# Optimization experiments

Measured on AMD Instinct MI355X. Metric: run time of the kernel, lower is better.

## Reference

```python
import jax, jax.numpy as jnp
import numpy as np

B, NPG, EPG = 32768, 50, 400  # graphs, nodes/graph, edges/graph
N, E = B * NPG, B * EPG
BN_EPS = 1e-5


def setup_inputs() -> dict:
    key = jax.random.key(0)
    ks = jax.random.split(key, 16)
    # block-structured edges: endpoints local to each graph, then offset
    local = jax.random.randint(ks[0], (2, B, EPG), 0, NPG)
    offs = (jnp.arange(B, dtype=jnp.int32) * NPG)[None, :, None]
    edge_index = (local.astype(jnp.int32) + offs).reshape(2, E)
    x = jax.random.normal(ks[1], (N, 1), dtype=jnp.float32)
    s = 0.3
    inp = {
        "x": x, "edge_index": edge_index,
        "W11": s * jax.random.normal(ks[2], (1, 4)), "b11": jnp.zeros(4),
        "W21": s * jax.random.normal(ks[3], (4, 4)), "b21": jnp.zeros(4),
        "W12": s * jax.random.normal(ks[4], (1, 4)), "b12": jnp.zeros(4),
        "W22": s * jax.random.normal(ks[5], (4, 4)), "b22": jnp.zeros(4),
        "W13": s * jax.random.normal(ks[6], (1, 4)), "b13": jnp.zeros(4),
        "W23": s * jax.random.normal(ks[7], (4, 4)), "b23": jnp.zeros(4),
        "fc1_w": 0.05 * jax.random.normal(ks[8], (600, 16)), "fc1_b": jnp.zeros(16),
        "bn1_g": jnp.ones(16), "bn1_b": jnp.zeros(16),
        "fc2_w": 0.2 * jax.random.normal(ks[9], (16, 32)), "fc2_b": jnp.zeros(32),
        "bn2_g": jnp.ones(32), "bn2_b": jnp.zeros(32),
        "fc3_w": 0.2 * jax.random.normal(ks[10], (32, 2)), "fc3_b": jnp.zeros(2),
    }
    return inp


def _gcn_norm(edge_index, n):
    # add self-loops, symmetric D^{-1/2} A_hat D^{-1/2} normalization (PyG GCNConv)
    loop = jnp.arange(n, dtype=edge_index.dtype)
    src = jnp.concatenate([edge_index[0], loop])
    dst = jnp.concatenate([edge_index[1], loop])
    deg = jax.ops.segment_sum(jnp.ones_like(src, dtype=jnp.float32), dst, num_segments=n)
    dinv = jax.lax.rsqrt(jnp.maximum(deg, 1.0))  # deg >= 1 via self-loop
    return src, dst, dinv[src] * dinv[dst]


def _gcn(x, W, b, src, dst, norm, n):
    h = x @ W                                  # [N, out]
    msg = h[src] * norm[:, None]               # gather + scale
    return jax.ops.segment_sum(msg, dst, num_segments=n) + b  # scatter-add


def _bn(h, g, b):
    m = jnp.mean(h, axis=0)
    v = jnp.var(h, axis=0)  # biased, matches torch BN training forward
    return (h - m) * jax.lax.rsqrt(v + BN_EPS) * g + b


def reference(x, edge_index, W11, b11, W21, b21, W12, b12, W22, b22,
              W13, b13, W23, b23, fc1_w, fc1_b, bn1_g, bn1_b,
              fc2_w, fc2_b, bn2_g, bn2_b, fc3_w, fc3_b):
    n = x.shape[0]
    src, dst, norm = _gcn_norm(edge_index, n)
    x1 = _gcn(_gcn(x, W11, b11, src, dst, norm, n), W21, b21, src, dst, norm, n)
    x2 = _gcn(_gcn(x, W12, b12, src, dst, norm, n), W22, b22, src, dst, norm, n)
    x3 = _gcn(_gcn(x, W13, b13, src, dst, norm, n), W23, b23, src, dst, norm, n)
    h = jnp.concatenate([x1, x2, x3], axis=-1)          # [N, 12]
    h = h.reshape(n // NPG, NPG * 12)                   # [B, 600]
    h = _bn(jax.nn.relu(h @ fc1_w + fc1_b), bn1_g, bn1_b)
    h = _bn(jax.nn.relu(h @ fc2_w + fc2_b), bn2_g, bn2_b)
    return h @ fc3_w + fc3_b                            # [B, 2] logits
```

## Files before the change

kernel.cpp:

```cpp
#include <hip/hip_runtime.h>

#define NPG 50
#define EPG 400
#define NGRAPH 32768
#define NNODE (NGRAPH * NPG)
#define NEDGE (NGRAPH * EPG)
#define BN_EPS 1e-5f

#define WS_A1T 0
#define WS_A2T 1280
#define WS_K0 2560
#define WS_ST1 2576
#define WS_W2 2608
#define WS_B2 3120
#define WS_ST2 3152
#define WS_W3 3216
#define WS_B3 3280
#define WS_CNT1 3282
#define WS_CNT2 3283
#define WS_H1 4096

__global__ void FullGCN_52286931861996_kernel() {}

struct Params12 { const float* p[12]; };

__device__ __forceinline__ float rdlane(float v, int s) {
    return __uint_as_float(__builtin_amdgcn_readlane(__float_as_uint(v), s));
}

__global__ void k0_pre(Params12 wp, const float* __restrict__ fc1w,
                       const float* __restrict__ fc1b, float* __restrict__ ws) {
    __shared__ float U[12], C[12], Bc[12];
    int tid = threadIdx.x;
    if (tid < 12) {
        int b = tid >> 2, j = tid & 3;
        const float* W1 = wp.p[b * 4 + 0];
        const float* b1 = wp.p[b * 4 + 1];
        const float* W2 = wp.p[b * 4 + 2];
        const float* b2 = wp.p[b * 4 + 3];
        float u = 0.f, c = 0.f;
        for (int k = 0; k < 4; k++) {
            float w2 = W2[k * 4 + j];
            u += W1[k] * w2;
            c += b1[k] * w2;
        }
        U[tid] = u; C[tid] = c; Bc[tid] = b2[j];
    }
    __syncthreads();
    for (int idx = tid; idx < 2560; idx += blockDim.x) {
        int which = (idx >= 1280);
        int e = which ? idx - 1280 : idx;
        int l = e / 20, k = e % 20;
        int o = l >> 2, n = (l & 3) + 4 * k;
        const float* V = which ? C : U;
        float a = 0.f;
        if (k < 13 && n < NPG)
            for (int f = 0; f < 12; f++) a += V[f] * fc1w[(n * 12 + f) * 16 + o];
        ws[idx] = a;
    }
    if (tid < 16) {
        float a = fc1b[tid];
        for (int n = 0; n < NPG; n++)
            for (int f = 0; f < 12; f++)
                a += Bc[f] * fc1w[(n * 12 + f) * 16 + tid];
        ws[WS_K0 + tid] = a;
    }
    if (tid < 32) ws[WS_ST1 + tid] = 0.f;
    if (tid >= 64 && tid < 128) ws[WS_ST2 + (tid - 64)] = 0.f;
    if (tid == 200) { ((unsigned int*)ws)[WS_CNT1] = 0u; ((unsigned int*)ws)[WS_CNT2] = 0u; }
}

#define GPB 4
#define CROWW 13
#define CALLOC 840
#define CZERO 168
__global__ __launch_bounds__(256) void k1_gcn(const float* __restrict__ x,
                                              const int* __restrict__ edges,
                                              const float* __restrict__ ws,
                                              float* __restrict__ h1) {
    __shared__ unsigned int sC[GPB][CALLOC];
    __shared__ float2 sOut[GPB][64];

    int tid = threadIdx.x;
    int w = tid >> 6, lane = tid & 63;
    int g = blockIdx.x * GPB + w;
    int nb = g * NPG;
    unsigned int* sCw = &sC[w][0];

    {
        uint4 z = make_uint4(0u, 0u, 0u, 0u);
        uint4* cz = (uint4*)sCw;
        #pragma unroll
        for (int i = 0; i < 3; i++) {
            int j = lane + i * 64;
            if (j < CZERO) cz[j] = z;
        }
    }

    float xv = (lane < NPG) ? x[nb + lane] : 0.f;

    const int4* s4 = (const int4*)edges;
    const int4* d4 = s4 + (NEDGE / 4);
    int base = g * (EPG / 4);
    int4 sa = s4[base + lane];
    int4 da = d4[base + lane];
    bool m2 = lane < (EPG / 4 - 64);
    int4 sb = make_int4(0, 0, 0, 0), db = make_int4(0, 0, 0, 0);
    if (m2) { sb = s4[base + 64 + lane]; db = d4[base + 64 + lane]; }

    {
        int sl[8], dl[8];
        sl[0] = sa.x - nb; sl[1] = sa.y - nb; sl[2] = sa.z - nb; sl[3] = sa.w - nb;
        dl[0] = da.x - nb; dl[1] = da.y - nb; dl[2] = da.z - nb; dl[3] = da.w - nb;
        sl[4] = sb.x - nb; sl[5] = sb.y - nb; sl[6] = sb.z - nb; sl[7] = sb.w - nb;
        dl[4] = db.x - nb; dl[5] = db.y - nb; dl[6] = db.z - nb; dl[7] = db.w - nb;
        #pragma unroll
        for (int e = 0; e < 4; e++) {
            int cell = dl[e] * 52 + sl[e];
            atomicAdd(&sCw[cell >> 2], 1u << ((cell & 3) * 8));
        }
        if (m2) {
            #pragma unroll
            for (int e = 4; e < 8; e++) {
                int cell = dl[e] * 52 + sl[e];
                atomicAdd(&sCw[cell >> 2], 1u << ((cell & 3) * 8));
            }
        }
    }

    unsigned int wv[13];
    #pragma unroll
    for (int k = 0; k < 13; k++) wv[k] = sCw[lane * CROWW + k];

    unsigned int acc2 = 0;
    #pragma unroll
    for (int k = 0; k < 13; k++)
        acc2 += (wv[k] & 0x00FF00FFu) + ((wv[k] >> 8) & 0x00FF00FFu);
    int deg = 1 + (int)((acc2 & 0xFFFFu) + (acc2 >> 16));
    float dinv = rsqrtf((float)deg);
    float dd = dinv * dinv;
    float vs = dinv * xv;

    float pxa = 0.f, ra = 0.f;
    #pragma unroll
    for (int s = 0; s < NPG; s++) {
        float cnt = (float)((wv[s >> 2] >> ((s & 3) * 8)) & 0xFFu);
        pxa += cnt * rdlane(vs, s);
        ra  += cnt * rdlane(dinv, s);
    }
    float px = dinv * pxa + dd * xv;
    float rr = dinv * ra + dd;

    float vs2 = dinv * px;
    float ppa = 0.f;
    #pragma unroll
    for (int s = 0; s < NPG; s++) {
        float cnt = (float)((wv[s >> 2] >> ((s & 3) * 8)) & 0xFFu);
        ppa += cnt * rdlane(vs2, s);
    }
    float ppx = dinv * ppa + dd * px;

    if (lane >= NPG) { ppx = 0.f; rr = 0.f; }
    sOut[w][lane] = make_float2(ppx, rr);

    const float4* a1v = (const float4*)(ws + lane * 20);
    const float4* a2v = (const float4*)(ws + 1280 + lane * 20);
    float4 c0 = a1v[0], c1 = a1v[1], c2 = a1v[2];
    float  c3 = ws[lane * 20 + 12];
    float4 d0 = a2v[0], d1 = a2v[1], d2 = a2v[2];
    float  d3 = ws[1280 + lane * 20 + 12];
    float k0v = ws[WS_K0 + (lane >> 2)];
    float A1r[13] = {c0.x, c0.y, c0.z, c0.w, c1.x, c1.y, c1.z, c1.w, c2.x, c2.y, c2.z, c2.w, c3};
    float A2r[13] = {d0.x, d0.y, d0.z, d0.w, d1.x, d1.y, d1.z, d1.w, d2.x, d2.y, d2.z, d2.w, d3};

    int o = lane >> 2, q = lane & 3;
    float accz = 0.f;
    #pragma unroll
    for (int k = 0; k < 13; k++) {
        float2 pr = sOut[w][q + 4 * k];
        accz += pr.x * A1r[k] + pr.y * A2r[k];
    }
    accz += __shfl_down(accz, 2, 4);
    accz += __shfl_down(accz, 1, 4);
    if (q == 0) h1[(size_t)g * 16 + o] = fmaxf(accz + k0v, 0.f);
}

__global__ __launch_bounds__(256) void k23_stats_fold(const float* __restrict__ h1,
                                                      const float* __restrict__ fc2w,
                                                      const float* __restrict__ fc2b,
                                                      const float* __restrict__ g1,
                                                      const float* __restrict__ b1,
                                                      float* __restrict__ ws) {
    __shared__ float ps[32];
    __shared__ int last;
    int tid = threadIdx.x;
    if (tid < 32) ps[tid] = 0.f;
    __syncthreads();
    int c = tid & 15;
    float s = 0.f, sq = 0.f;
    for (int i = blockIdx.x * blockDim.x + tid; i < NGRAPH * 16; i += gridDim.x * blockDim.x) {
        float v = h1[i];
        s += v; sq += v * v;
    }
    s += __shfl_xor(s, 16); s += __shfl_xor(s, 32);
    sq += __shfl_xor(sq, 16); sq += __shfl_xor(sq, 32);
    if ((tid & 63) < 16) {
        atomicAdd(&ps[c], s);
        atomicAdd(&ps[16 + c], sq);
    }
    __syncthreads();
    if (tid < 32) atomicAdd(&ws[WS_ST1 + tid], ps[tid]);
    __threadfence();
    if (tid == 0)
        last = (atomicAdd(&((unsigned int*)ws)[WS_CNT1], 1u) == (unsigned int)(gridDim.x - 1));
    __syncthreads();
    if (!last) return;
    __threadfence();
    __shared__ float s1[16], t1[16];
    if (tid < 16) {
        float m  = atomicAdd(&ws[WS_ST1 + tid], 0.f) / (float)NGRAPH;
        float v  = atomicAdd(&ws[WS_ST1 + 16 + tid], 0.f) / (float)NGRAPH - m * m;
        float sc = g1[tid] * rsqrtf(v + BN_EPS);
        s1[tid] = sc;
        t1[tid] = b1[tid] - m * sc;
    }
    __syncthreads();
    for (int idx = tid; idx < 512; idx += blockDim.x)
        ws[WS_W2 + idx] = s1[idx >> 5] * fc2w[idx];
    if (tid < 32) {
        float a = fc2b[tid];
        for (int i = 0; i < 16; i++) a += t1[i] * fc2w[i * 32 + tid];
        ws[WS_B2 + tid] = a;
    }
}

__global__ __launch_bounds__(256) void k45_fc2_fold(const float* __restrict__ h1,
                                                    const float* __restrict__ fc3w,
                                                    const float* __restrict__ fc3b,
                                                    const float* __restrict__ g2,
                                                    const float* __restrict__ b2g,
                                                    float* __restrict__ ws) {
    __shared__ float w2[512];
    __shared__ float b2[32];
    __shared__ float pSum[32], pSq[32];
    __shared__ int last;
    int tid = threadIdx.x;
    for (int i = tid; i < 512; i += 256) w2[i] = ws[WS_W2 + i];
    if (tid < 32) {
        b2[tid] = ws[WS_B2 + tid];
        pSum[tid] = 0.f;
        pSq[tid] = 0.f;
    }
    __syncthreads();
    int g = blockIdx.x * blockDim.x + tid;
    int lane = tid & 63;
    const float4* h4 = (const float4*)(h1 + (size_t)g * 16);
    float4 a0 = h4[0], a1 = h4[1], a2 = h4[2], a3 = h4[3];
    float hin[16] = {a0.x, a0.y, a0.z, a0.w, a1.x, a1.y, a1.z, a1.w,
                     a2.x, a2.y, a2.z, a2.w, a3.x, a3.y, a3.z, a3.w};
    for (int o = 0; o < 32; o++) {
        float acc = b2[o];
        #pragma unroll
        for (int i = 0; i < 16; i++) acc += hin[i] * w2[i * 32 + o];
        acc = fmaxf(acc, 0.f);
        float v = acc, v2 = acc * acc;
        #pragma unroll
        for (int off = 32; off; off >>= 1) {
            v += __shfl_xor(v, off);
            v2 += __shfl_xor(v2, off);
        }
        if (lane == 0) {
            atomicAdd(&pSum[o], v);
            atomicAdd(&pSq[o], v2);
        }
    }
    __syncthreads();
    if (tid < 32) {
        atomicAdd(&ws[WS_ST2 + tid], pSum[tid]);
        atomicAdd(&ws[WS_ST2 + 32 + tid], pSq[tid]);
    }
    __threadfence();
    if (tid == 0)
        last = (atomicAdd(&((unsigned int*)ws)[WS_CNT2], 1u) == (unsigned int)(gridDim.x - 1));
    __syncthreads();
    if (!last) return;
    __threadfence();
    __shared__ float s2[32], t2[32];
    if (tid < 32) {
        float m  = atomicAdd(&ws[WS_ST2 + tid], 0.f) / (float)NGRAPH;
        float v  = atomicAdd(&ws[WS_ST2 + 32 + tid], 0.f) / (float)NGRAPH - m * m;
        float sc = g2[tid] * rsqrtf(v + BN_EPS);
        s2[tid] = sc;
        t2[tid] = b2g[tid] - m * sc;
    }
    __syncthreads();
    if (tid < 64) ws[WS_W3 + tid] = s2[tid >> 1] * fc3w[tid];
    if (tid < 2) {
        float a = fc3b[tid];
        for (int i = 0; i < 32; i++) a += t2[i] * fc3w[i * 2 + tid];
        ws[WS_B3 + tid] = a;
    }
}

__global__ __launch_bounds__(256) void k6_out(const float* __restrict__ h1,
                                              const float* __restrict__ ws,
                                              float2* __restrict__ out) {
    __shared__ float w2[512];
    __shared__ float b2[32];
    __shared__ float w3[64];
    __shared__ float b3[2];
    int tid = threadIdx.x;
    for (int i = tid; i < 512; i += 256) w2[i] = ws[WS_W2 + i];
    if (tid < 32) b2[tid] = ws[WS_B2 + tid];
    if (tid >= 64 && tid < 128) w3[tid - 64] = ws[WS_W3 + (tid - 64)];
    if (tid >= 128 && tid < 130) b3[tid - 128] = ws[WS_B3 + (tid - 128)];
    __syncthreads();
    int g = blockIdx.x * blockDim.x + tid;
    const float4* h4 = (const float4*)(h1 + (size_t)g * 16);
    float4 a0 = h4[0], a1 = h4[1], a2 = h4[2], a3 = h4[3];
    float hin[16] = {a0.x, a0.y, a0.z, a0.w, a1.x, a1.y, a1.z, a1.w,
                     a2.x, a2.y, a2.z, a2.w, a3.x, a3.y, a3.z, a3.w};
    float z0 = b3[0], z1 = b3[1];
    for (int o = 0; o < 32; o++) {
        float acc = b2[o];
        #pragma unroll
        for (int i = 0; i < 16; i++) acc += hin[i] * w2[i * 32 + o];
        acc = fmaxf(acc, 0.f);
        z0 += acc * w3[o * 2];
        z1 += acc * w3[o * 2 + 1];
    }
    out[g] = make_float2(z0, z1);
}

extern "C" void kernel_launch(void* const* d_in, const int* in_sizes, int n_in,
                              void* d_out, int out_size, void* d_ws, size_t ws_size,
                              hipStream_t stream) {
    (void)in_sizes; (void)n_in; (void)out_size; (void)ws_size;
    const float* x = (const float*)d_in[0];
    const int* edges = (const int*)d_in[1];
    Params12 wp;
    for (int i = 0; i < 12; i++) wp.p[i] = (const float*)d_in[2 + i];
    const float* fc1w = (const float*)d_in[14];
    const float* fc1b = (const float*)d_in[15];
    const float* bn1g = (const float*)d_in[16];
    const float* bn1b = (const float*)d_in[17];
    const float* fc2w = (const float*)d_in[18];
    const float* fc2b = (const float*)d_in[19];
    const float* bn2g = (const float*)d_in[20];
    const float* bn2b = (const float*)d_in[21];
    const float* fc3w = (const float*)d_in[22];
    const float* fc3b = (const float*)d_in[23];

    float* ws = (float*)d_ws;
    float* h1 = ws + WS_H1;

    k0_pre<<<1, 256, 0, stream>>>(wp, fc1w, fc1b, ws);
    k1_gcn<<<NGRAPH / GPB, 256, 0, stream>>>(x, edges, ws, h1);
    k23_stats_fold<<<256, 256, 0, stream>>>(h1, fc2w, fc2b, bn1g, bn1b, ws);
    k45_fc2_fold<<<NGRAPH / 256, 256, 0, stream>>>(h1, fc3w, fc3b, bn2g, bn2b, ws);
    k6_out<<<NGRAPH / 256, 256, 0, stream>>>(h1, ws, (float2*)d_out);
}
```

Measured before the change: 275.9 us.

## Fuse fc2 stats and output kernels via grid barrier; use LDS broadcast in GCN

Merges the fc2 BN-stats kernel and the final output kernel into a single launch. The last block to arrive computes the folded fc3 weights, and the other blocks spin on a counter flag before reading them. This removes one kernel launch and keeps h1 and w2 resident in registers. In the GCN kernel, the per-source lane reads (rdlane) are replaced by LDS broadcast reads, and the A-matrix loads are hoisted ahead of the edge processing. The spin barrier relies on all 128 blocks being co-resident, which holds at this grid size but adds a deadlock risk.

New measurement: 279.3 us. No clear change (+1.2%).

```diff
diff --git a/kernel.cpp b/kernel.cpp
--- a/kernel.cpp
+++ b/kernel.cpp
@@ -99,70 +99,6 @@
 
     float xv = (lane < NPG) ? x[nb + lane] : 0.f;
 
-    const int4* s4 = (const int4*)edges;
-    const int4* d4 = s4 + (NEDGE / 4);
-    int base = g * (EPG / 4);
-    int4 sa = s4[base + lane];
-    int4 da = d4[base + lane];
-    bool m2 = lane < (EPG / 4 - 64);
-    int4 sb = make_int4(0, 0, 0, 0), db = make_int4(0, 0, 0, 0);
-    if (m2) { sb = s4[base + 64 + lane]; db = d4[base + 64 + lane]; }
-
-    {
-        int sl[8], dl[8];
-        sl[0] = sa.x - nb; sl[1] = sa.y - nb; sl[2] = sa.z - nb; sl[3] = sa.w - nb;
-        dl[0] = da.x - nb; dl[1] = da.y - nb; dl[2] = da.z - nb; dl[3] = da.w - nb;
-        sl[4] = sb.x - nb; sl[5] = sb.y - nb; sl[6] = sb.z - nb; sl[7] = sb.w - nb;
-        dl[4] = db.x - nb; dl[5] = db.y - nb; dl[6] = db.z - nb; dl[7] = db.w - nb;
-        #pragma unroll
-        for (int e = 0; e < 4; e++) {
-            int cell = dl[e] * 52 + sl[e];
-            atomicAdd(&sCw[cell >> 2], 1u << ((cell & 3) * 8));
-        }
-        if (m2) {
-            #pragma unroll
-            for (int e = 4; e < 8; e++) {
-                int cell = dl[e] * 52 + sl[e];
-                atomicAdd(&sCw[cell >> 2], 1u << ((cell & 3) * 8));
-            }
-        }
-    }
-
-    unsigned int wv[13];
-    #pragma unroll
-    for (int k = 0; k < 13; k++) wv[k] = sCw[lane * CROWW + k];
-
-    unsigned int acc2 = 0;
-    #pragma unroll
-    for (int k = 0; k < 13; k++)
-        acc2 += (wv[k] & 0x00FF00FFu) + ((wv[k] >> 8) & 0x00FF00FFu);
-    int deg = 1 + (int)((acc2 & 0xFFFFu) + (acc2 >> 16));
-    float dinv = rsqrtf((float)deg);
-    float dd = dinv * dinv;
-    float vs = dinv * xv;
-
-    float pxa = 0.f, ra = 0.f;
-    #pragma unroll
-    for (int s = 0; s < NPG; s++) {
-        float cnt = (float)((wv[s >> 2] >> ((s & 3) * 8)) & 0xFFu);
-        pxa += cnt * rdlane(vs, s);
-        ra  += cnt * rdlane(dinv, s);
-    }
-    float px = dinv * pxa + dd * xv;
-    float rr = dinv * ra + dd;
-
-    float vs2 = dinv * px;
-    float ppa = 0.f;
-    #pragma unroll
-    for (int s = 0; s < NPG; s++) {
-        float cnt = (float)((wv[s >> 2] >> ((s & 3) * 8)) & 0xFFu);
-        ppa += cnt * rdlane(vs2, s);
-    }
-    float ppx = dinv * ppa + dd * px;
-
-    if (lane >= NPG) { ppx = 0.f; rr = 0.f; }
-    sOut[w][lane] = make_float2(ppx, rr);
-
     const float4* a1v = (const float4*)(ws + lane * 20);
     const float4* a2v = (const float4*)(ws + 1280 + lane * 20);
     float4 c0 = a1v[0], c1 = a1v[1], c2 = a1v[2];
@@ -172,6 +108,73 @@
     float k0v = ws[WS_K0 + (lane >> 2)];
     float A1r[13] = {c0.x, c0.y, c0.z, c0.w, c1.x, c1.y, c1.z, c1.w, c2.x, c2.y, c2.z, c2.w, c3};
     float A2r[13] = {d0.x, d0.y, d0.z, d0.w, d1.x, d1.y, d1.z, d1.w, d2.x, d2.y, d2.z, d2.w, d3};
+
+    const int4* s4 = (const int4*)edges;
+    const int4* d4 = s4 + (NEDGE / 4);
+    int base = g * (EPG / 4);
+    int4 sa = s4[base + lane];
+    int4 da = d4[base + lane];
+    bool m2 = lane < (EPG / 4 - 64);
+    int4 sb = make_int4(0, 0, 0, 0), db = make_int4(0, 0, 0, 0);
+    if (m2) { sb = s4[base + 64 + lane]; db = d4[base + 64 + lane]; }
+
+    {
+        int sl[8], dl[8];
+        sl[0] = sa.x - nb; sl[1] = sa.y - nb; sl[2] = sa.z - nb; sl[3] = sa.w - nb;
+        dl[0] = da.x - nb; dl[1] = da.y - nb; dl[2] = da.z - nb; dl[3] = da.w - nb;
+        sl[4] = sb.x - nb; sl[5] = sb.y - nb; sl[6] = sb.z - nb; sl[7] = sb.w - nb;
+        dl[4] = db.x - nb; dl[5] = db.y - nb; dl[6] = db.z - nb; dl[7] = db.w - nb;
+        #pragma unroll
+        for (int e = 0; e < 4; e++) {
+            int cell = dl[e] * 52 + sl[e];
+            atomicAdd(&sCw[cell >> 2], 1u << ((cell & 3) * 8));
+        }
+        if (m2) {
+            #pragma unroll
+            for (int e = 4; e < 8; e++) {
+                int cell = dl[e] * 52 + sl[e];
+                atomicAdd(&sCw[cell >> 2], 1u << ((cell & 3) * 8));
+            }
+        }
+    }
+
+    unsigned int wv[13];
+    #pragma unroll
+    for (int k = 0; k < 13; k++) wv[k] = sCw[lane * CROWW + k];
+
+    unsigned int acc2 = 0;
+    #pragma unroll
+    for (int k = 0; k < 13; k++)
+        acc2 += (wv[k] & 0x00FF00FFu) + ((wv[k] >> 8) & 0x00FF00FFu);
+    int deg = 1 + (int)((acc2 & 0xFFFFu) + (acc2 >> 16));
+    float dinv = rsqrtf((float)deg);
+    float dd = dinv * dinv;
+    float vs = dinv * xv;
+
+    sOut[w][lane] = make_float2(vs, dinv);
+    float pxa = 0.f, ra = 0.f;
+    #pragma unroll
+    for (int s = 0; s < NPG; s++) {
+        float cnt = (float)((wv[s >> 2] >> ((s & 3) * 8)) & 0xFFu);
+        float2 vd = sOut[w][s];
+        pxa += cnt * vd.x;
+        ra  += cnt * vd.y;
+    }
+    float px = dinv * pxa + dd * xv;
+    float rr = dinv * ra + dd;
+
+    float vs2 = dinv * px;
+    sOut[w][lane].x = vs2;
+    float ppa = 0.f;
+    #pragma unroll
+    for (int s = 0; s < NPG; s++) {
+        float cnt = (float)((wv[s >> 2] >> ((s & 3) * 8)) & 0xFFu);
+        ppa += cnt * sOut[w][s].x;
+    }
+    float ppx = dinv * ppa + dd * px;
+
+    if (lane >= NPG) { ppx = 0.f; rr = 0.f; }
+    sOut[w][lane] = make_float2(ppx, rr);
 
     int o = lane >> 2, q = lane & 3;
     float accz = 0.f;
@@ -234,16 +237,18 @@
     }
 }
 
-__global__ __launch_bounds__(256) void k45_fc2_fold(const float* __restrict__ h1,
-                                                    const float* __restrict__ fc3w,
-                                                    const float* __restrict__ fc3b,
-                                                    const float* __restrict__ g2,
-                                                    const float* __restrict__ b2g,
-                                                    float* __restrict__ ws) {
+__global__ __launch_bounds__(256) void k456_fc2_fold_out(const float* __restrict__ h1,
+                                                         const float* __restrict__ fc3w,
+                                                         const float* __restrict__ fc3b,
+                                                         const float* __restrict__ g2,
+                                                         const float* __restrict__ b2g,
+                                                         float* __restrict__ ws,
+                                                         float2* __restrict__ out) {
     __shared__ float w2[512];
     __shared__ float b2[32];
     __shared__ float pSum[32], pSq[32];
-    __shared__ int last;
+    __shared__ unsigned int amF;
+    unsigned int* cnt2 = &((unsigned int*)ws)[WS_CNT2];
     int tid = threadIdx.x;
     for (int i = tid; i < 512; i += 256) w2[i] = ws[WS_W2 + i];
     if (tid < 32) {
@@ -281,45 +286,36 @@
     }
     __threadfence();
     if (tid == 0)
-        last = (atomicAdd(&((unsigned int*)ws)[WS_CNT2], 1u) == (unsigned int)(gridDim.x - 1));
-    __syncthreads();
-    if (!last) return;
-    __threadfence();
-    __shared__ float s2[32], t2[32];
-    if (tid < 32) {
-        float m  = atomicAdd(&ws[WS_ST2 + tid], 0.f) / (float)NGRAPH;
-        float v  = atomicAdd(&ws[WS_ST2 + 32 + tid], 0.f) / (float)NGRAPH - m * m;
-        float sc = g2[tid] * rsqrtf(v + BN_EPS);
-        s2[tid] = sc;
-        t2[tid] = b2g[tid] - m * sc;
-    }
-    __syncthreads();
-    if (tid < 64) ws[WS_W3 + tid] = s2[tid >> 1] * fc3w[tid];
-    if (tid < 2) {
-        float a = fc3b[tid];
-        for (int i = 0; i < 32; i++) a += t2[i] * fc3w[i * 2 + tid];
-        ws[WS_B3 + tid] = a;
-    }
-}
-
-__global__ __launch_bounds__(256) void k6_out(const float* __restrict__ h1,
-                                              const float* __restrict__ ws,
-                                              float2* __restrict__ out) {
-    __shared__ float w2[512];
-    __shared__ float b2[32];
-    __shared__ float w3[64];
-    __shared__ float b3[2];
-    int tid = threadIdx.x;
-    for (int i = tid; i < 512; i += 256) w2[i] = ws[WS_W2 + i];
-    if (tid < 32) b2[tid] = ws[WS_B2 + tid];
-    if (tid >= 64 && tid < 128) w3[tid - 64] = ws[WS_W3 + (tid - 64)];
-    if (tid >= 128 && tid < 130) b3[tid - 128] = ws[WS_B3 + (tid - 128)];
-    __syncthreads();
-    int g = blockIdx.x * blockDim.x + tid;
-    const float4* h4 = (const float4*)(h1 + (size_t)g * 16);
-    float4 a0 = h4[0], a1 = h4[1], a2 = h4[2], a3 = h4[3];
-    float hin[16] = {a0.x, a0.y, a0.z, a0.w, a1.x, a1.y, a1.z, a1.w,
-                     a2.x, a2.y, a2.z, a2.w, a3.x, a3.y, a3.z, a3.w};
+        amF = (atomicAdd(cnt2, 1u) == (unsigned int)(gridDim.x - 1)) ? 1u : 0u;
+    __syncthreads();
+    if (amF) {
+        __shared__ float s2[32], t2[32];
+        if (tid < 32) {
+            float m  = atomicAdd(&ws[WS_ST2 + tid], 0.f) / (float)NGRAPH;
+            float v  = atomicAdd(&ws[WS_ST2 + 32 + tid], 0.f) / (float)NGRAPH - m * m;
+            float sc = g2[tid] * rsqrtf(v + BN_EPS);
+            s2[tid] = sc;
+            t2[tid] = b2g[tid] - m * sc;
+        }
+        __syncthreads();
+        if (tid < 64)
+            atomicExch((unsigned int*)&ws[WS_W3 + tid], __float_as_uint(s2[tid >> 1] * fc3w[tid]));
+        if (tid >= 64 && tid < 66) {
+            int j = tid - 64;
+            float a = fc3b[j];
+            for (int i = 0; i < 32; i++) a += t2[i] * fc3w[i * 2 + j];
+            atomicExch((unsigned int*)&ws[WS_B3 + j], __float_as_uint(a));
+        }
+        __threadfence();
+        if (tid == 0) atomicAdd(cnt2, 0x10000u);
+    }
+    if (tid == 0) { while ((atomicAdd(cnt2, 0u) >> 16) == 0u) { } }
+    __syncthreads();
+    __shared__ float w3[64], b3[2];
+    if (tid < 64) w3[tid] = __uint_as_float(atomicAdd((unsigned int*)&ws[WS_W3 + tid], 0u));
+    if (tid >= 64 && tid < 66)
+        b3[tid - 64] = __uint_as_float(atomicAdd((unsigned int*)&ws[WS_B3 + (tid - 64)], 0u));
+    __syncthreads();
     float z0 = b3[0], z1 = b3[1];
     for (int o = 0; o < 32; o++) {
         float acc = b2[o];
@@ -357,6 +353,6 @@
     k0_pre<<<1, 256, 0, stream>>>(wp, fc1w, fc1b, ws);
     k1_gcn<<<NGRAPH / GPB, 256, 0, stream>>>(x, edges, ws, h1);
     k23_stats_fold<<<256, 256, 0, stream>>>(h1, fc2w, fc2b, bn1g, bn1b, ws);
-    k45_fc2_fold<<<NGRAPH / 256, 256, 0, stream>>>(h1, fc3w, fc3b, bn2g, bn2b, ws);
-    k6_out<<<NGRAPH / 256, 256, 0, stream>>>(h1, ws, (float2*)d_out);
-}
+    k456_fc2_fold_out<<<NGRAPH / 256, 256, 0, stream>>>(h1, fc3w, fc3b, bn2g, bn2b, ws,
+                                                        (float2*)d_out);
+}
```
